# Optimization experiments

Hardware: AMD Instinct MI355X
Metric: run time of the kernel (lower is better)

Reference implementation:

```python
import jax, jax.numpy as jnp
import numpy as np
from jax import lax

DIM = 128
K = 3
PAD = K // 2


def setup_inputs() -> dict:
    key = jax.random.key(0)
    k1, k2, k3, k4, k5 = jax.random.split(key, 5)
    B, H, W = 64, 32, 32
    wdim = DIM * DIM * K * K + DIM  # 147584
    # scale question_rep (it encodes conv weights) for numerical sanity
    question_rep = jax.random.normal(k1, (B, wdim), dtype=jnp.float32) * 0.05
    lhs_rep = jax.random.normal(k2, (B, DIM, H, W), dtype=jnp.float32)
    rhs_rep = jax.random.normal(k3, (B, DIM, H, W), dtype=jnp.float32)
    proj_w = jax.random.normal(k4, (DIM, 2 * DIM), dtype=jnp.float32) * (1.0 / np.sqrt(2 * DIM))
    proj_b = jax.random.normal(k5, (DIM,), dtype=jnp.float32) * 0.01
    return {"question_rep": question_rep, "lhs_rep": lhs_rep,
            "rhs_rep": rhs_rep, "proj_w": proj_w, "proj_b": proj_b}


def _per_sample_conv(x, w, b):
    # x: [dim, H, W], w: [dim, dim, K, K], b: [dim]
    y = lax.conv_general_dilated(
        x[None], w, window_strides=(1, 1),
        padding=[(PAD, PAD), (PAD, PAD)],
        dimension_numbers=("NCHW", "OIHW", "NCHW"))
    return y[0] + b[:, None, None]


def reference(question_rep, lhs_rep, rhs_rep, proj_w, proj_b):
    B = question_rep.shape[0]
    wdim = DIM * DIM * K * K
    cnn_weight = question_rep[:, :wdim].reshape(B, DIM, DIM, K, K)
    cnn_bias = question_rep[:, wdim:]  # [B, dim]
    # 1x1 projection conv: cat along channels then contract
    cat = jnp.concatenate([lhs_rep, rhs_rep], axis=1)  # [B, 2*dim, H, W]
    cnn_inp = jnp.einsum("bchw,oc->bohw", cat, proj_w) + proj_b[None, :, None, None]
    # per-sample dynamic conv, vectorized over batch (equiv. grouped conv)
    out = jax.vmap(_per_sample_conv)(cnn_inp, cnn_weight, cnn_bias)
    return out
```

## Files before the change

### kernel.cpp

```cpp
#include <hip/hip_runtime.h>
#include <hip/hip_bf16.h>

#define QSTRIDE 147584
#define WOFF    147456

typedef __attribute__((ext_vector_type(8))) short bf16x8;
typedef __attribute__((ext_vector_type(4))) float f32x4;

static __device__ __forceinline__ ushort f2bf(float f) {
  union { float f; unsigned u; } x; x.f = f;
  unsigned r = x.u + 0x7fffu + ((x.u >> 16) & 1u);
  return (ushort)(r >> 16);
}
static __device__ __forceinline__ unsigned pk2(ushort a, ushort b) {
  return (unsigned)a | ((unsigned)b << 16);
}
static __device__ __forceinline__ void async16(const ushort* g, ushort* l) {
  __builtin_amdgcn_global_load_lds((const __attribute__((address_space(1))) void*)g,
                                   (__attribute__((address_space(3))) void*)l, 16, 0, 0);
}

__global__ __launch_bounds__(256) void pack_w_kernel(const float* __restrict__ q,
                                                     ushort* __restrict__ wt2) {
  __shared__ float Ls[4608];
  int b = blockIdx.x >> 3, ogrp = blockIdx.x & 7;
  int t = threadIdx.x;
  const float* gbase = q + (size_t)b * QSTRIDE + (size_t)ogrp * 16 * 1152;
  ushort* dstb = wt2 + (size_t)b * 147456;
  int o_loc = t >> 6;
  int ci    = (t & 63) * 2;
  int cq    = ci >> 5, coff = ci & 31;
  for (int r = 0; r < 4; ++r) {
    __syncthreads();
    const float* gs = gbase + r * 4608;
#pragma unroll
    for (int i = 0; i < 18; ++i) Ls[i * 256 + t] = gs[i * 256 + t];
    __syncthreads();
    int o_full = ogrp * 16 + r * 4 + o_loc;
    const float* v = Ls + o_loc * 1152 + ci * 9;
    float a[18];
#pragma unroll
    for (int i = 0; i < 18; ++i) a[i] = v[i];
    ushort* dd = dstb + (size_t)cq * 4096 + o_full * 32 + coff;
#pragma unroll
    for (int tap = 0; tap < 9; ++tap) {
      unsigned pkv = pk2(f2bf(a[tap]), f2bf(a[9 + tap]));
      *(unsigned*)(dd + (size_t)tap * 16384) = pkv;
    }
  }
}

__global__ __launch_bounds__(256) void pack_pw_kernel(const float* __restrict__ pw,
                                                      ushort* __restrict__ pwb2) {
  int tg = blockIdx.x * 256 + threadIdx.x;
  int o  = tg >> 5;
  int c0 = (tg & 31) * 8;
  const float4* s4 = (const float4*)(pw + (size_t)o * 256 + c0);
  float4 f0 = s4[0], f1 = s4[1];
  uint4 pkv;
  pkv.x = pk2(f2bf(f0.x), f2bf(f0.y)); pkv.y = pk2(f2bf(f0.z), f2bf(f0.w));
  pkv.z = pk2(f2bf(f1.x), f2bf(f1.y)); pkv.w = pk2(f2bf(f1.z), f2bf(f1.w));
  *(uint4*)(pwb2 + (size_t)(c0 >> 5) * 4096 + o * 32 + (c0 & 31)) = pkv;
}

__global__ __launch_bounds__(256) void zero_border_kernel(ushort* __restrict__ xp2) {
  int b = blockIdx.x, t = threadIdx.x;
  for (int idx = t; idx < 528; idx += 256) {
    int cq = idx / 132, r = idx - cq * 132;
    int hp, wp;
    if (r < 34)       { hp = 0;        wp = r; }
    else if (r < 68)  { hp = 33;       wp = r - 34; }
    else if (r < 100) { hp = r - 67;   wp = 0; }
    else              { hp = r - 99;   wp = 33; }
    uint4 z = {0u,0u,0u,0u};
    uint4* dst = (uint4*)(xp2 + (((size_t)b * 4 + cq) * 1156 + hp * 34 + wp) * 32);
#pragma unroll
    for (int i = 0; i < 4; ++i) dst[i] = z;
  }
}

__global__ __launch_bounds__(256, 2) void proj_kernel(const ushort* __restrict__ pwb2,
                                                      const float* __restrict__ lhs,
                                                      const float* __restrict__ rhs,
                                                      const float* __restrict__ pb,
                                                      ushort* __restrict__ xp2) {
  __shared__ ushort As[2][4096];
  __shared__ ushort Bs[4096];
  int b = blockIdx.y, tile = blockIdx.x;
  int p0 = tile * 128;
  int t = threadIdx.x;
  int lane = t & 63, wv = t >> 6;
  int m0 = (wv & 1) * 64, n0 = (wv >> 1) * 64;
  int quad = lane >> 4, li = lane & 15;
  f32x4 acc[4][4] = {};
  int cgrp = t & 3;
  int pq   = t >> 2;

  const float* base_l = lhs + (size_t)b * 131072 + (size_t)(cgrp * 8) * 1024 + p0 + 2 * pq;
  const float* base_r = rhs + (size_t)b * 131072 + (size_t)(cgrp * 8) * 1024 + p0 + 2 * pq;

#define PROJ_DMA(c, buf) do { \
    const ushort* ag_ = pwb2 + (size_t)(c) * 4096; \
    async16(ag_ + (size_t)wv * 512 + lane * 8,       As[buf] + wv * 512); \
    async16(ag_ + (size_t)(wv + 4) * 512 + lane * 8, As[buf] + (wv + 4) * 512); \
  } while (0)

#define PROJ_LOAD(c, fb) do { \
    const float* src_ = ((c) < 4 ? base_l : base_r) + (size_t)(((c) & 3) * 32) * 1024; \
    _Pragma("unroll") \
    for (int j = 0; j < 8; ++j) fb[j] = *(const float2*)(src_ + (size_t)j * 1024); \
  } while (0)

#define PROJ_PACK(fb) do { \
    pk0.x = pk2(f2bf(fb[0].x), f2bf(fb[1].x)); \
    pk0.y = pk2(f2bf(fb[2].x), f2bf(fb[3].x)); \
    pk0.z = pk2(f2bf(fb[4].x), f2bf(fb[5].x)); \
    pk0.w = pk2(f2bf(fb[6].x), f2bf(fb[7].x)); \
    pk1.x = pk2(f2bf(fb[0].y), f2bf(fb[1].y)); \
    pk1.y = pk2(f2bf(fb[2].y), f2bf(fb[3].y)); \
    pk1.z = pk2(f2bf(fb[4].y), f2bf(fb[5].y)); \
    pk1.w = pk2(f2bf(fb[6].y), f2bf(fb[7].y)); \
  } while (0)

  float2 fb0[8], fb1[8];
  PROJ_DMA(0, 0);
  PROJ_LOAD(0, fb0);

#pragma unroll
  for (int c = 0; c < 8; ++c) {
    uint4 pk0, pk1;
    if (c & 1) PROJ_PACK(fb1); else PROJ_PACK(fb0);
    asm volatile("s_waitcnt lgkmcnt(0)" ::: "memory");
    __builtin_amdgcn_s_barrier();
    *(uint4*)(Bs + (size_t)(2*pq)   * 32 + cgrp * 8) = pk0;
    *(uint4*)(Bs + (size_t)(2*pq+1) * 32 + cgrp * 8) = pk1;
    __syncthreads();
    if (c < 7) {
      PROJ_DMA(c + 1, (c + 1) & 1);
      if (c & 1) PROJ_LOAD(c + 1, fb0); else PROJ_LOAD(c + 1, fb1);
    }
    const ushort* ar = As[c & 1];
    bf16x8 af[4], bg[4];
#pragma unroll
    for (int mi = 0; mi < 4; ++mi)
      af[mi] = *(const bf16x8*)(ar + (m0 + mi*16 + li) * 32 + quad * 8);
#pragma unroll
    for (int ni = 0; ni < 4; ++ni)
      bg[ni] = *(const bf16x8*)(Bs + (n0 + ni*16 + li) * 32 + quad * 8);
#pragma unroll
    for (int mi = 0; mi < 4; ++mi)
#pragma unroll
      for (int ni = 0; ni < 4; ++ni)
        acc[mi][ni] = __builtin_amdgcn_mfma_f32_16x16x32_bf16(af[mi], bg[ni], acc[mi][ni], 0, 0, 0);
  }

  ushort* xpb = xp2 + (size_t)b * 4 * 1156 * 32;
#pragma unroll
  for (int mi = 0; mi < 4; ++mi) {
    int o0 = m0 + mi*16 + quad*4;
    float4 bias = *(const float4*)(pb + o0);
#pragma unroll
    for (int ni = 0; ni < 4; ++ni) {
      int p = p0 + n0 + ni*16 + li;
      int h = p >> 5, w = p & 31;
      ushort* dp = xpb + ((size_t)(o0 >> 5) * 1156 + (h + 1) * 34 + (w + 1)) * 32 + (o0 & 31);
      f32x4 a = acc[mi][ni];
      uint2 pkv;
      pkv.x = pk2(f2bf(a.x + bias.x), f2bf(a.y + bias.y));
      pkv.y = pk2(f2bf(a.z + bias.z), f2bf(a.w + bias.w));
      *(uint2*)dp = pkv;
    }
  }
#undef PROJ_DMA
#undef PROJ_LOAD
#undef PROJ_PACK
}

__global__ __launch_bounds__(256, 2) void conv_kernel(const ushort* __restrict__ wt2,
                                                      const ushort* __restrict__ xp2,
                                                      const float* __restrict__ q,
                                                      float* __restrict__ out) {
  __shared__ ushort As[2][4096];
  __shared__ ushort Bs[6528];
  int blk = blockIdx.x;
  int b = blk & 63, tile = blk >> 6;
  int p0 = tile * 128, h0 = tile * 4;
  int t = threadIdx.x;
  int lane = t & 63, wv = t >> 6;
  int m0 = (wv & 1) * 64, n0 = (wv >> 1) * 64;
  int quad = lane >> 4, li = lane & 15;
  f32x4 acc[4][4] = {};
  const ushort* wtb = wt2 + (size_t)b * 147456;
  const ushort* xpb = xp2 + (size_t)b * 147968;

  for (int cq = 0; cq < 4; ++cq) {
    __syncthreads();
    {
      const ushort* bgp = xpb + (size_t)(cq * 1156 + h0 * 34) * 32;
#pragma unroll
      for (int p = 0; p < 3; ++p)
        async16(bgp + (size_t)(p * 256 + t) * 8, Bs + p * 2048 + wv * 512);
      if (t < 48)
        async16(bgp + (size_t)(768 + t) * 8, Bs + 6144);
    }
    {
      const ushort* ag = wtb + (size_t)cq * 4096;
      async16(ag + (size_t)t * 8,         As[0] + wv * 512);
      async16(ag + (size_t)(256 + t) * 8, As[0] + 2048 + wv * 512);
    }
    for (int tap = 0; tap < 9; ++tap) {
      __syncthreads();
      if (tap < 8) {
        const ushort* ag = wtb + (size_t)((tap + 1) * 4 + cq) * 4096;
        ushort* ab = As[(tap + 1) & 1];
        async16(ag + (size_t)t * 8,         ab + wv * 512);
        async16(ag + (size_t)(256 + t) * 8, ab + 2048 + wv * 512);
      }
      int kh = tap / 3, kw = tap - kh * 3;
      const ushort* ar = As[tap & 1];
      bf16x8 af[4], bg[4];
#pragma unroll
      for (int mi = 0; mi < 4; ++mi)
        af[mi] = *(const bf16x8*)(ar + (m0 + mi*16 + li) * 32 + quad * 8);
#pragma unroll
      for (int ni = 0; ni < 4; ++ni) {
        int pl = n0 + ni*16 + li;
        int h = pl >> 5, w = pl & 31;
        bg[ni] = *(const bf16x8*)(Bs + ((h + kh) * 34 + (w + kw)) * 32 + quad * 8);
      }
#pragma unroll
      for (int mi = 0; mi < 4; ++mi)
#pragma unroll
        for (int ni = 0; ni < 4; ++ni)
          acc[mi][ni] = __builtin_amdgcn_mfma_f32_16x16x32_bf16(af[mi], bg[ni], acc[mi][ni], 0, 0, 0);
    }
  }

  const float* qb = q + (size_t)b * QSTRIDE + WOFF;
  float* ob = out + (size_t)b * 128 * 1024 + p0;
#pragma unroll
  for (int mi = 0; mi < 4; ++mi) {
    int o0 = m0 + mi*16 + quad*4;
    float4 bias = *(const float4*)(qb + o0);
#pragma unroll
    for (int ni = 0; ni < 4; ++ni) {
      int pl = n0 + ni*16 + li;
      float* dp = ob + (size_t)o0 * 1024 + pl;
      f32x4 a = acc[mi][ni];
      dp[0]    = a.x + bias.x;
      dp[1024] = a.y + bias.y;
      dp[2048] = a.z + bias.z;
      dp[3072] = a.w + bias.w;
    }
  }
}

extern "C" void kernel_launch(void* const* d_in, const int* in_sizes, int n_in,
                              void* d_out, int out_size, void* d_ws, size_t ws_size,
                              hipStream_t stream) {
  const float* q   = (const float*)d_in[0];
  const float* lhs = (const float*)d_in[1];
  const float* rhs = (const float*)d_in[2];
  const float* pw  = (const float*)d_in[3];
  const float* pb  = (const float*)d_in[4];
  float* out = (float*)d_out;

  char* ws = (char*)d_ws;
  ushort* wt2  = (ushort*)(ws);
  ushort* pwb2 = (ushort*)(ws + 18874368);
  ushort* xp2  = (ushort*)(ws + 18939904);

  pack_w_kernel     <<<512, 256, 0, stream>>>(q, wt2);
  pack_pw_kernel    <<<16,  256, 0, stream>>>(pw, pwb2);
  zero_border_kernel<<<64,  256, 0, stream>>>(xp2);
  proj_kernel       <<<dim3(8, 64), 256, 0, stream>>>(pwb2, lhs, rhs, pb, xp2);
  conv_kernel       <<<512, 256, 0, stream>>>(wt2, xp2, q, out);
}
```

Measured before the change: 182.2 us.

## Deepen proj and conv pipelines with triple-buffered A and double-buffered B

Both the projection GEMM and the per-sample conv kernel now keep two weight tiles in flight with a triple-buffered A in LDS. The conv input tile B is double-buffered and prefetched partway through the previous channel group's taps. Single combined waits on vmcnt/lgkmcnt plus a barrier replace the paired __syncthreads per step, and the conv loop is fully unrolled. This is meant to hide global-to-LDS latency and cut barrier stalls, at the cost of more LDS per block, which could lower occupancy, and of hand-tuned vmcnt counts that must match the issued loads exactly.

After: 177.7 us. -2.5%, faster.

```diff
diff --git a/kernel.cpp b/kernel.cpp
--- a/kernel.cpp
+++ b/kernel.cpp
@@ -19,6 +19,10 @@
   __builtin_amdgcn_global_load_lds((const __attribute__((address_space(1))) void*)g,
                                    (__attribute__((address_space(3))) void*)l, 16, 0, 0);
 }
+
+#define WAITBAR_(vm) asm volatile("s_waitcnt vmcnt(" #vm ") lgkmcnt(0)\n\ts_barrier" ::: "memory")
+#define WAITBAR(vm) WAITBAR_(vm)
+#define BARSYNC() asm volatile("s_waitcnt lgkmcnt(0)\n\ts_barrier" ::: "memory")
 
 __global__ __launch_bounds__(256) void pack_w_kernel(const float* __restrict__ q,
                                                      ushort* __restrict__ wt2) {
@@ -84,8 +88,8 @@
                                                       const float* __restrict__ rhs,
                                                       const float* __restrict__ pb,
                                                       ushort* __restrict__ xp2) {
-  __shared__ ushort As[2][4096];
-  __shared__ ushort Bs[4096];
+  __shared__ ushort As[3][4096];
+  __shared__ ushort Bs[2][4096];
   int b = blockIdx.y, tile = blockIdx.x;
   int p0 = tile * 128;
   int t = threadIdx.x;
@@ -99,60 +103,63 @@
   const float* base_l = lhs + (size_t)b * 131072 + (size_t)(cgrp * 8) * 1024 + p0 + 2 * pq;
   const float* base_r = rhs + (size_t)b * 131072 + (size_t)(cgrp * 8) * 1024 + p0 + 2 * pq;
 
+  float2 fb[3][8];
+
 #define PROJ_DMA(c, buf) do { \
     const ushort* ag_ = pwb2 + (size_t)(c) * 4096; \
-    async16(ag_ + (size_t)wv * 512 + lane * 8,       As[buf] + wv * 512); \
-    async16(ag_ + (size_t)(wv + 4) * 512 + lane * 8, As[buf] + (wv + 4) * 512); \
+    async16(ag_ + (size_t)wv * 512 + lane * 8,       &As[buf][0] + wv * 512); \
+    async16(ag_ + (size_t)(wv + 4) * 512 + lane * 8, &As[buf][0] + (wv + 4) * 512); \
   } while (0)
 
-#define PROJ_LOAD(c, fb) do { \
+#define PROJ_LOAD(c, sl) do { \
     const float* src_ = ((c) < 4 ? base_l : base_r) + (size_t)(((c) & 3) * 32) * 1024; \
     _Pragma("unroll") \
-    for (int j = 0; j < 8; ++j) fb[j] = *(const float2*)(src_ + (size_t)j * 1024); \
+    for (int j = 0; j < 8; ++j) fb[sl][j] = *(const float2*)(src_ + (size_t)j * 1024); \
   } while (0)
 
-#define PROJ_PACK(fb) do { \
-    pk0.x = pk2(f2bf(fb[0].x), f2bf(fb[1].x)); \
-    pk0.y = pk2(f2bf(fb[2].x), f2bf(fb[3].x)); \
-    pk0.z = pk2(f2bf(fb[4].x), f2bf(fb[5].x)); \
-    pk0.w = pk2(f2bf(fb[6].x), f2bf(fb[7].x)); \
-    pk1.x = pk2(f2bf(fb[0].y), f2bf(fb[1].y)); \
-    pk1.y = pk2(f2bf(fb[2].y), f2bf(fb[3].y)); \
-    pk1.z = pk2(f2bf(fb[4].y), f2bf(fb[5].y)); \
-    pk1.w = pk2(f2bf(fb[6].y), f2bf(fb[7].y)); \
-  } while (0)
-
-  float2 fb0[8], fb1[8];
-  PROJ_DMA(0, 0);
-  PROJ_LOAD(0, fb0);
+  PROJ_DMA(0, 0); PROJ_LOAD(0, 0);
+  PROJ_DMA(1, 1); PROJ_LOAD(1, 1);
 
 #pragma unroll
   for (int c = 0; c < 8; ++c) {
+    const int sl = c % 3;
     uint4 pk0, pk1;
-    if (c & 1) PROJ_PACK(fb1); else PROJ_PACK(fb0);
-    asm volatile("s_waitcnt lgkmcnt(0)" ::: "memory");
-    __builtin_amdgcn_s_barrier();
-    *(uint4*)(Bs + (size_t)(2*pq)   * 32 + cgrp * 8) = pk0;
-    *(uint4*)(Bs + (size_t)(2*pq+1) * 32 + cgrp * 8) = pk1;
-    __syncthreads();
-    if (c < 7) {
-      PROJ_DMA(c + 1, (c + 1) & 1);
-      if (c & 1) PROJ_LOAD(c + 1, fb0); else PROJ_LOAD(c + 1, fb1);
-    }
-    const ushort* ar = As[c & 1];
+    pk0.x = pk2(f2bf(fb[sl][0].x), f2bf(fb[sl][1].x));
+    pk0.y = pk2(f2bf(fb[sl][2].x), f2bf(fb[sl][3].x));
+    pk0.z = pk2(f2bf(fb[sl][4].x), f2bf(fb[sl][5].x));
+    pk0.w = pk2(f2bf(fb[sl][6].x), f2bf(fb[sl][7].x));
+    pk1.x = pk2(f2bf(fb[sl][0].y), f2bf(fb[sl][1].y));
+    pk1.y = pk2(f2bf(fb[sl][2].y), f2bf(fb[sl][3].y));
+    pk1.z = pk2(f2bf(fb[sl][4].y), f2bf(fb[sl][5].y));
+    pk1.w = pk2(f2bf(fb[sl][6].y), f2bf(fb[sl][7].y));
+    {
+      ushort* bw = &Bs[c & 1][0];
+      *(uint4*)(bw + (size_t)(2*pq)   * 32 + cgrp * 8) = pk0;
+      *(uint4*)(bw + (size_t)(2*pq+1) * 32 + cgrp * 8) = pk1;
+    }
+    BARSYNC();
+    if (c < 6) {
+      PROJ_DMA(c + 2, (c + 2) % 3);
+      PROJ_LOAD(c + 2, (c + 2) % 3);
+    }
+    __builtin_amdgcn_sched_barrier(0);
+    const ushort* ar = &As[c % 3][0];
+    const ushort* br = &Bs[c & 1][0];
     bf16x8 af[4], bg[4];
 #pragma unroll
     for (int mi = 0; mi < 4; ++mi)
       af[mi] = *(const bf16x8*)(ar + (m0 + mi*16 + li) * 32 + quad * 8);
 #pragma unroll
     for (int ni = 0; ni < 4; ++ni)
-      bg[ni] = *(const bf16x8*)(Bs + (n0 + ni*16 + li) * 32 + quad * 8);
+      bg[ni] = *(const bf16x8*)(br + (n0 + ni*16 + li) * 32 + quad * 8);
 #pragma unroll
     for (int mi = 0; mi < 4; ++mi)
 #pragma unroll
       for (int ni = 0; ni < 4; ++ni)
         acc[mi][ni] = __builtin_amdgcn_mfma_f32_16x16x32_bf16(af[mi], bg[ni], acc[mi][ni], 0, 0, 0);
   }
+#undef PROJ_DMA
+#undef PROJ_LOAD
 
   ushort* xpb = xp2 + (size_t)b * 4 * 1156 * 32;
 #pragma unroll
@@ -171,17 +178,14 @@
       *(uint2*)dp = pkv;
     }
   }
-#undef PROJ_DMA
-#undef PROJ_LOAD
-#undef PROJ_PACK
 }
 
 __global__ __launch_bounds__(256, 2) void conv_kernel(const ushort* __restrict__ wt2,
                                                       const ushort* __restrict__ xp2,
                                                       const float* __restrict__ q,
                                                       float* __restrict__ out) {
-  __shared__ ushort As[2][4096];
-  __shared__ ushort Bs[6528];
+  __shared__ ushort As[3][4096];
+  __shared__ ushort Bs[2][6528];
   int blk = blockIdx.x;
   int b = blk & 63, tile = blk >> 6;
   int p0 = tile * 128, h0 = tile * 4;
@@ -193,48 +197,61 @@
   const ushort* wtb = wt2 + (size_t)b * 147456;
   const ushort* xpb = xp2 + (size_t)b * 147968;
 
-  for (int cq = 0; cq < 4; ++cq) {
-    __syncthreads();
-    {
-      const ushort* bgp = xpb + (size_t)(cq * 1156 + h0 * 34) * 32;
-#pragma unroll
-      for (int p = 0; p < 3; ++p)
-        async16(bgp + (size_t)(p * 256 + t) * 8, Bs + p * 2048 + wv * 512);
-      if (t < 48)
-        async16(bgp + (size_t)(768 + t) * 8, Bs + 6144);
-    }
-    {
-      const ushort* ag = wtb + (size_t)cq * 4096;
-      async16(ag + (size_t)t * 8,         As[0] + wv * 512);
-      async16(ag + (size_t)(256 + t) * 8, As[0] + 2048 + wv * 512);
-    }
-    for (int tap = 0; tap < 9; ++tap) {
-      __syncthreads();
-      if (tap < 8) {
-        const ushort* ag = wtb + (size_t)((tap + 1) * 4 + cq) * 4096;
-        ushort* ab = As[(tap + 1) & 1];
-        async16(ag + (size_t)t * 8,         ab + wv * 512);
-        async16(ag + (size_t)(256 + t) * 8, ab + 2048 + wv * 512);
-      }
-      int kh = tap / 3, kw = tap - kh * 3;
-      const ushort* ar = As[tap & 1];
-      bf16x8 af[4], bg[4];
-#pragma unroll
-      for (int mi = 0; mi < 4; ++mi)
-        af[mi] = *(const bf16x8*)(ar + (m0 + mi*16 + li) * 32 + quad * 8);
-#pragma unroll
-      for (int ni = 0; ni < 4; ++ni) {
-        int pl = n0 + ni*16 + li;
-        int h = pl >> 5, w = pl & 31;
-        bg[ni] = *(const bf16x8*)(Bs + ((h + kh) * 34 + (w + kw)) * 32 + quad * 8);
-      }
-#pragma unroll
-      for (int mi = 0; mi < 4; ++mi)
-#pragma unroll
-        for (int ni = 0; ni < 4; ++ni)
-          acc[mi][ni] = __builtin_amdgcn_mfma_f32_16x16x32_bf16(af[mi], bg[ni], acc[mi][ni], 0, 0, 0);
-    }
-  }
+  auto stageA = [&](int tapi, int cqi, int buf) {
+    const ushort* ag = wtb + (size_t)(tapi * 4 + cqi) * 4096;
+    async16(ag + (size_t)t * 8,         &As[buf][0] + wv * 512);
+    async16(ag + (size_t)(256 + t) * 8, &As[buf][0] + 2048 + wv * 512);
+  };
+  auto stageB = [&](int cqi, int buf) {
+    const ushort* bgp = xpb + (size_t)(cqi * 1156 + h0 * 34) * 32;
+    int lb = wv * 204;
+    async16(bgp + (size_t)(lb +       lane) * 8, &Bs[buf][0] + (lb      ) * 8);
+    async16(bgp + (size_t)(lb +  64 + lane) * 8, &Bs[buf][0] + (lb +  64) * 8);
+    async16(bgp + (size_t)(lb + 128 + lane) * 8, &Bs[buf][0] + (lb + 128) * 8);
+    if (lane < 12)
+      async16(bgp + (size_t)(lb + 192 + lane) * 8, &Bs[buf][0] + (lb + 192) * 8);
+  };
+
+  stageB(0, 0);
+  stageA(0, 0, 0);
+  stageA(1, 0, 1);
+
+#define CSTEP(cq, tap, vm) do { \
+    WAITBAR(vm); \
+    if (9*(cq)+(tap)+2 <= 35) \
+      stageA((9*(cq)+(tap)+2) % 9, (9*(cq)+(tap)+2) / 9, ((tap)+2) % 3); \
+    if ((tap) == 6 && (cq) < 3) stageB((cq)+1, ((cq)+1) & 1); \
+    __builtin_amdgcn_sched_barrier(0); \
+    { const ushort* ar = &As[(tap) % 3][0]; \
+      const ushort* br = &Bs[(cq) & 1][0]; \
+      const int kh_ = (tap) / 3, kw_ = (tap) % 3; \
+      bf16x8 af[4], bg[4]; \
+      _Pragma("unroll") \
+      for (int mi = 0; mi < 4; ++mi) \
+        af[mi] = *(const bf16x8*)(ar + (m0 + mi*16 + li) * 32 + quad * 8); \
+      _Pragma("unroll") \
+      for (int ni = 0; ni < 4; ++ni) { \
+        int pl = n0 + ni*16 + li; \
+        int hh = pl >> 5, ww = pl & 31; \
+        bg[ni] = *(const bf16x8*)(br + ((hh + kh_) * 34 + (ww + kw_)) * 32 + quad * 8); \
+      } \
+      _Pragma("unroll") \
+      for (int mi = 0; mi < 4; ++mi) \
+        _Pragma("unroll") \
+        for (int ni = 0; ni < 4; ++ni) \
+          acc[mi][ni] = __builtin_amdgcn_mfma_f32_16x16x32_bf16(af[mi], bg[ni], acc[mi][ni], 0, 0, 0); \
+    } \
+  } while (0)
+
+  CSTEP(0,0,2); CSTEP(0,1,2); CSTEP(0,2,2); CSTEP(0,3,2); CSTEP(0,4,2);
+  CSTEP(0,5,2); CSTEP(0,6,2); CSTEP(0,7,6); CSTEP(0,8,6);
+  CSTEP(1,0,2); CSTEP(1,1,2); CSTEP(1,2,2); CSTEP(1,3,2); CSTEP(1,4,2);
+  CSTEP(1,5,2); CSTEP(1,6,2); CSTEP(1,7,6); CSTEP(1,8,6);
+  CSTEP(2,0,2); CSTEP(2,1,2); CSTEP(2,2,2); CSTEP(2,3,2); CSTEP(2,4,2);
+  CSTEP(2,5,2); CSTEP(2,6,2); CSTEP(2,7,6); CSTEP(2,8,6);
+  CSTEP(3,0,2); CSTEP(3,1,2); CSTEP(3,2,2); CSTEP(3,3,2); CSTEP(3,4,2);
+  CSTEP(3,5,2); CSTEP(3,6,2); CSTEP(3,7,2); CSTEP(3,8,0);
+#undef CSTEP
 
   const float* qb = q + (size_t)b * QSTRIDE + WOFF;
   float* ob = out + (size_t)b * 128 * 1024 + p0;
```
